# Performance work log

Measured on AMD Instinct MI355X. Metric: run time of the kernel, lower is better.

The kernel has to match this reference:

```python
import jax, jax.numpy as jnp
import numpy as np

NUM_HEADS = 12
QK_SCALE = 1.0
EPS = 1e-12  # torch.nn.functional.normalize default eps


def _l2norm(t):
    # matches torch F.normalize: x / max(||x||_2, eps) along last axis
    n = jnp.sqrt(jnp.sum(t * t, axis=-1, keepdims=True))
    return t / jnp.maximum(n, EPS)


def setup_inputs() -> dict:
    key = jax.random.key(0)
    k1, k2 = jax.random.split(key)
    B, N, dim = 8, 4096, 768
    x = jax.random.normal(k1, (B, N, 3 * dim), dtype=jnp.float32)
    temperature = jnp.ones((NUM_HEADS, 1, 1), dtype=jnp.float32)
    proj_w = jax.random.normal(k2, (dim, dim), dtype=jnp.float32) * (1.0 / np.sqrt(dim))
    proj_b = jnp.zeros((dim,), dtype=jnp.float32)
    return {"x": x, "temperature": temperature, "proj_w": proj_w, "proj_b": proj_b}


def reference(x, temperature, proj_w, proj_b):
    B, N, C3 = x.shape
    C = C3 // 3
    H = NUM_HEADS
    d = C // H
    # (B, N, 3, H, d) -> (3, B, H, N, d)
    qkv = x.reshape(B, N, 3, H, d).transpose(2, 0, 3, 1, 4)
    q, k, v = qkv[0], qkv[1], qkv[2]
    q = jnp.swapaxes(q, -2, -1) * QK_SCALE   # [B, H, d, N]
    v = jnp.swapaxes(v, -2, -1)              # [B, H, d, N]
    q = _l2norm(q)                           # normalize over tokens N
    k = _l2norm(k)                           # normalize over head dim d (k is [B,H,N,d])
    # cross-covariance attention over channels: [B, H, d, d]
    attn = jnp.einsum('bhdn,bhne->bhde', q, k) * temperature
    attn = jax.nn.softmax(attn, axis=-1)
    out = jnp.einsum('bhde,bhen->bhdn', attn, v)  # [B, H, d, N]
    out = out.transpose(0, 3, 1, 2).reshape(B, N, C)  # [B, N, C]
    out = out @ proj_w.T + proj_b
    return out
```

## Files before the change

### kernel.cpp

```cpp
#include <hip/hip_runtime.h>
#include <hip/hip_bf16.h>

#define BB 8
#define NN 4096
#define HH 12
#define CC 768
#define C3 2304

typedef float  f32x4  __attribute__((ext_vector_type(4)));
typedef __bf16 bf16x8 __attribute__((ext_vector_type(8)));
typedef __bf16 bf16x4 __attribute__((ext_vector_type(4)));

__device__ __forceinline__ void gload16(const void* g, void* l) {
  __builtin_amdgcn_global_load_lds((const __attribute__((address_space(1))) void*)g,
                                   (__attribute__((address_space(3))) void*)l, 16, 0, 0);
}

__global__ __launch_bounds__(256) void k1_logits(const float* __restrict__ x,
                                                 __bf16* __restrict__ vb,
                                                 float* __restrict__ Spart,
                                                 float* __restrict__ Qpart) {
  const int slice = blockIdx.x;
  const int h = blockIdx.y, b = blockIdx.z;
  const int tid = threadIdx.x;
  __shared__ __bf16 qT[64][40];
  __shared__ __bf16 kT[64][40];
  __shared__ float  qws[4][64];

  const int t   = tid >> 3;
  const int sub = tid & 7;
  const int w   = tid >> 6, lane = tid & 63;
  const int fr  = lane & 15, fk = lane >> 4;

  const float* qbase = x + (size_t)(b * NN + slice * 512) * C3 + h * 64 + sub * 8;
  __bf16* vbase = vb + (size_t)(b * NN + slice * 512) * CC + h * 64 + sub * 8;

  float qss8[8];
#pragma unroll
  for (int j = 0; j < 8; ++j) qss8[j] = 0.f;
  f32x4 acc[4];
#pragma unroll
  for (int tn = 0; tn < 4; ++tn) acc[tn] = (f32x4){0.f, 0.f, 0.f, 0.f};

  for (int step = 0; step < 16; ++step) {
    const float* qp = qbase + (size_t)(step * 32 + t) * C3;
    const float4 q0 = *(const float4*)(qp);
    const float4 q1 = *(const float4*)(qp + 4);
    const float4 k0 = *(const float4*)(qp + 768);
    const float4 k1 = *(const float4*)(qp + 772);
    const float4 v0 = *(const float4*)(qp + 1536);
    const float4 v1 = *(const float4*)(qp + 1540);
    float ss = k0.x * k0.x + k0.y * k0.y + k0.z * k0.z + k0.w * k0.w +
               k1.x * k1.x + k1.y * k1.y + k1.z * k1.z + k1.w * k1.w;
    ss += __shfl_xor(ss, 1);
    ss += __shfl_xor(ss, 2);
    ss += __shfl_xor(ss, 4);
    const float inv = 1.0f / fmaxf(sqrtf(ss), 1e-12f);
    bf16x8 vv;
    vv[0] = (__bf16)v0.x; vv[1] = (__bf16)v0.y; vv[2] = (__bf16)v0.z; vv[3] = (__bf16)v0.w;
    vv[4] = (__bf16)v1.x; vv[5] = (__bf16)v1.y; vv[6] = (__bf16)v1.z; vv[7] = (__bf16)v1.w;
    *(bf16x8*)(vbase + (size_t)(step * 32 + t) * CC) = vv;
    __syncthreads();
    const int c0 = sub * 8;
    qT[c0 + 0][t] = (__bf16)q0.x; qT[c0 + 1][t] = (__bf16)q0.y;
    qT[c0 + 2][t] = (__bf16)q0.z; qT[c0 + 3][t] = (__bf16)q0.w;
    qT[c0 + 4][t] = (__bf16)q1.x; qT[c0 + 5][t] = (__bf16)q1.y;
    qT[c0 + 6][t] = (__bf16)q1.z; qT[c0 + 7][t] = (__bf16)q1.w;
    kT[c0 + 0][t] = (__bf16)(k0.x * inv); kT[c0 + 1][t] = (__bf16)(k0.y * inv);
    kT[c0 + 2][t] = (__bf16)(k0.z * inv); kT[c0 + 3][t] = (__bf16)(k0.w * inv);
    kT[c0 + 4][t] = (__bf16)(k1.x * inv); kT[c0 + 5][t] = (__bf16)(k1.y * inv);
    kT[c0 + 6][t] = (__bf16)(k1.z * inv); kT[c0 + 7][t] = (__bf16)(k1.w * inv);
    qss8[0] = fmaf(q0.x, q0.x, qss8[0]); qss8[1] = fmaf(q0.y, q0.y, qss8[1]);
    qss8[2] = fmaf(q0.z, q0.z, qss8[2]); qss8[3] = fmaf(q0.w, q0.w, qss8[3]);
    qss8[4] = fmaf(q1.x, q1.x, qss8[4]); qss8[5] = fmaf(q1.y, q1.y, qss8[5]);
    qss8[6] = fmaf(q1.z, q1.z, qss8[6]); qss8[7] = fmaf(q1.w, q1.w, qss8[7]);
    __syncthreads();
    const bf16x8 afr = *(const bf16x8*)&qT[w * 16 + fr][fk * 8];
#pragma unroll
    for (int tn = 0; tn < 4; ++tn) {
      const bf16x8 bfr = *(const bf16x8*)&kT[tn * 16 + fr][fk * 8];
      acc[tn] = __builtin_amdgcn_mfma_f32_16x16x32_bf16(afr, bfr, acc[tn], 0, 0, 0);
    }
  }

  const int bh = b * HH + h;
  float* Sp = Spart + ((size_t)(slice * 96 + bh)) * 4096;
#pragma unroll
  for (int tn = 0; tn < 4; ++tn)
#pragma unroll
    for (int rr = 0; rr < 4; ++rr)
      Sp[(w * 16 + fk * 4 + rr) * 64 + tn * 16 + fr] = acc[tn][rr];

#pragma unroll
  for (int j = 0; j < 8; ++j) {
    float v = qss8[j];
    v += __shfl_xor(v, 8);
    v += __shfl_xor(v, 16);
    v += __shfl_xor(v, 32);
    if (lane < 8) qws[w][lane * 8 + j] = v;
  }
  __syncthreads();
  if (tid < 64) {
    const float qs = qws[0][tid] + qws[1][tid] + qws[2][tid] + qws[3][tid];
    Qpart[((size_t)(slice * 96 + bh)) * 64 + tid] = qs;
  }
}

__global__ __launch_bounds__(256) void k2_softmax(const float* __restrict__ Spart,
                                                  const float* __restrict__ Qpart,
                                                  const float* __restrict__ temp,
                                                  float* __restrict__ attn) {
  const int h = blockIdx.x, b = blockIdx.y;
  const int tid = threadIdx.x;
  const int i  = tid >> 2;
  const int qq = tid & 3;
  const int bh = b * HH + h;
  float qs = 0.f;
#pragma unroll
  for (int s = 0; s < 8; ++s) qs += Qpart[((size_t)(s * 96 + bh)) * 64 + i];
  float v[16];
#pragma unroll
  for (int j = 0; j < 16; ++j) v[j] = 0.f;
  for (int s = 0; s < 8; ++s) {
    const float* Sp = Spart + ((size_t)(s * 96 + bh)) * 4096 + i * 64 + qq * 16;
#pragma unroll
    for (int j = 0; j < 16; j += 4) {
      const float4 t4 = *(const float4*)(Sp + j);
      v[j] += t4.x; v[j + 1] += t4.y; v[j + 2] += t4.z; v[j + 3] += t4.w;
    }
  }
  const float rqs = 1.0f / fmaxf(sqrtf(qs), 1e-12f);
  const float tp  = temp[h] * rqs;
  float m = -3.4e38f;
#pragma unroll
  for (int j = 0; j < 16; ++j) { v[j] *= tp; m = fmaxf(m, v[j]); }
  m = fmaxf(m, __shfl_xor(m, 1));
  m = fmaxf(m, __shfl_xor(m, 2));
  float s = 0.f;
#pragma unroll
  for (int j = 0; j < 16; ++j) { v[j] = __expf(v[j] - m); s += v[j]; }
  s += __shfl_xor(s, 1);
  s += __shfl_xor(s, 2);
  const float inv = 1.0f / s;
  float* Ap = attn + (size_t)bh * 4096 + i * 64 + qq * 16;
#pragma unroll
  for (int j = 0; j < 16; j += 4) {
    float4 o;
    o.x = v[j] * inv; o.y = v[j + 1] * inv; o.z = v[j + 2] * inv; o.w = v[j + 3] * inv;
    *(float4*)(Ap + j) = o;
  }
}

__global__ __launch_bounds__(256) void k3_w2(const float* __restrict__ attn,
                                             const float* __restrict__ pw,
                                             __bf16* __restrict__ W2) {
  const int ct = blockIdx.x, h = blockIdx.y, b = blockIdx.z;
  const int co0 = ct * 64;
  __shared__ float pT[64][65];
  __shared__ float ab[64][64];
  const int tid = threadIdx.x;
  const int r = tid >> 2, c0 = (tid & 3) * 16;
  {
    const float* pp = pw + (size_t)(co0 + r) * CC + h * 64 + c0;
    const float4 p0 = *(const float4*)(pp + 0);
    const float4 p1 = *(const float4*)(pp + 4);
    const float4 p2 = *(const float4*)(pp + 8);
    const float4 p3 = *(const float4*)(pp + 12);
    const float* ap = attn + (size_t)(b * HH + h) * 4096 + r * 64 + c0;
    const float4 a0 = *(const float4*)(ap + 0);
    const float4 a1 = *(const float4*)(ap + 4);
    const float4 a2 = *(const float4*)(ap + 8);
    const float4 a3 = *(const float4*)(ap + 12);
    pT[c0 +  0][r] = p0.x; pT[c0 +  1][r] = p0.y; pT[c0 +  2][r] = p0.z; pT[c0 +  3][r] = p0.w;
    pT[c0 +  4][r] = p1.x; pT[c0 +  5][r] = p1.y; pT[c0 +  6][r] = p1.z; pT[c0 +  7][r] = p1.w;
    pT[c0 +  8][r] = p2.x; pT[c0 +  9][r] = p2.y; pT[c0 + 10][r] = p2.z; pT[c0 + 11][r] = p2.w;
    pT[c0 + 12][r] = p3.x; pT[c0 + 13][r] = p3.y; pT[c0 + 14][r] = p3.z; pT[c0 + 15][r] = p3.w;
    *(float4*)&ab[r][c0 + 0]  = a0;
    *(float4*)&ab[r][c0 + 4]  = a1;
    *(float4*)&ab[r][c0 + 8]  = a2;
    *(float4*)&ab[r][c0 + 12] = a3;
  }
  __syncthreads();
  const int col = tid & 63, jg = tid >> 6;
  float accJ[16];
#pragma unroll
  for (int c = 0; c < 16; ++c) accJ[c] = 0.f;
#pragma unroll 4
  for (int i = 0; i < 64; ++i) {
    const float p = pT[i][col];
    const float4* a4 = (const float4*)&ab[i][jg * 16];
    const float4 A0 = a4[0], A1 = a4[1], A2 = a4[2], A3 = a4[3];
    accJ[0]  = fmaf(p, A0.x, accJ[0]);  accJ[1]  = fmaf(p, A0.y, accJ[1]);
    accJ[2]  = fmaf(p, A0.z, accJ[2]);  accJ[3]  = fmaf(p, A0.w, accJ[3]);
    accJ[4]  = fmaf(p, A1.x, accJ[4]);  accJ[5]  = fmaf(p, A1.y, accJ[5]);
    accJ[6]  = fmaf(p, A1.z, accJ[6]);  accJ[7]  = fmaf(p, A1.w, accJ[7]);
    accJ[8]  = fmaf(p, A2.x, accJ[8]);  accJ[9]  = fmaf(p, A2.y, accJ[9]);
    accJ[10] = fmaf(p, A2.z, accJ[10]); accJ[11] = fmaf(p, A2.w, accJ[11]);
    accJ[12] = fmaf(p, A3.x, accJ[12]); accJ[13] = fmaf(p, A3.y, accJ[13]);
    accJ[14] = fmaf(p, A3.z, accJ[14]); accJ[15] = fmaf(p, A3.w, accJ[15]);
  }
  bf16x8 u0, u1;
#pragma unroll
  for (int c = 0; c < 8; ++c) { u0[c] = (__bf16)accJ[c]; u1[c] = (__bf16)accJ[8 + c]; }
  __bf16* wp = W2 + ((size_t)b * CC + co0 + col) * CC + h * 64 + jg * 16;
  *(bf16x8*)(wp)     = u0;
  *(bf16x8*)(wp + 8) = u1;
}

__global__ __launch_bounds__(256) void k4_gemm(const __bf16* __restrict__ vb,
                                               const __bf16* __restrict__ W2,
                                               const float* __restrict__ pb,
                                               float* __restrict__ out) {
  int id = blockIdx.x;
  const int bz = id / 192;
  const int rem = id - bz * 192;
  const int mg = rem / 48;
  const int idx = rem - mg * 48;
  const int nt = idx >> 3;
  const int mt = mg * 8 + (idx & 7);
  const int m0 = mt * 128, co0 = nt * 128;

  __shared__ __bf16 At[128][32];
  __shared__ __bf16 Bt[128][32];

  const int tid  = threadIdx.x;
  const int w    = tid >> 6, lane = tid & 63;
  const int wm   = w >> 1,   wn   = w & 1;
  const int fr   = lane & 15;
  const int fk   = lane >> 4;

  f32x4 acc[4][4];
#pragma unroll
  for (int tm = 0; tm < 4; ++tm)
#pragma unroll
    for (int tn = 0; tn < 4; ++tn) acc[tm][tn] = (f32x4){0.f, 0.f, 0.f, 0.f};

  const int srow = lane >> 2;
  const int scol = (lane & 3) * 8;
  const __bf16* Ag = vb + (size_t)(bz * NN + m0 + w * 32 + srow) * CC + scol;
  const __bf16* Bg = W2 + ((size_t)bz * CC + co0 + w * 32 + srow) * CC + scol;
  __bf16* lA0 = &At[w * 32][0];
  __bf16* lA1 = &At[w * 32 + 16][0];
  __bf16* lB0 = &Bt[w * 32][0];
  __bf16* lB1 = &Bt[w * 32 + 16][0];

  for (int kk = 0; kk < 24; ++kk) {
    const int kb = kk * 32;
    __syncthreads();
    gload16(Ag + kb,            lA0);
    gload16(Ag + 16 * CC + kb,  lA1);
    gload16(Bg + kb,            lB0);
    gload16(Bg + 16 * CC + kb,  lB1);
    __syncthreads();
    bf16x8 afr[4], bfr[4];
#pragma unroll
    for (int tm = 0; tm < 4; ++tm)
      afr[tm] = *(const bf16x8*)&At[wm * 64 + tm * 16 + fr][fk * 8];
#pragma unroll
    for (int tn = 0; tn < 4; ++tn)
      bfr[tn] = *(const bf16x8*)&Bt[wn * 64 + tn * 16 + fr][fk * 8];
#pragma unroll
    for (int tm = 0; tm < 4; ++tm)
#pragma unroll
      for (int tn = 0; tn < 4; ++tn)
        acc[tm][tn] = __builtin_amdgcn_mfma_f32_16x16x32_bf16(afr[tm], bfr[tn],
                                                              acc[tm][tn], 0, 0, 0);
  }

#pragma unroll
  for (int tn = 0; tn < 4; ++tn) {
    const int co = co0 + wn * 64 + tn * 16 + fr;
    const float bias = pb[co];
#pragma unroll
    for (int tm = 0; tm < 4; ++tm) {
#pragma unroll
      for (int rr = 0; rr < 4; ++rr) {
        const int row = m0 + wm * 64 + tm * 16 + fk * 4 + rr;
        out[(size_t)(bz * NN + row) * CC + co] = acc[tm][tn][rr] + bias;
      }
    }
  }
}

extern "C" void kernel_launch(void* const* d_in, const int* in_sizes, int n_in,
                              void* d_out, int out_size, void* d_ws, size_t ws_size,
                              hipStream_t stream) {
  const float* x    = (const float*)d_in[0];
  const float* temp = (const float*)d_in[1];
  const float* pw   = (const float*)d_in[2];
  const float* pb   = (const float*)d_in[3];
  float* out = (float*)d_out;
  char* ws = (char*)d_ws;

  float*  Spart = (float*)(ws);
  float*  Qpart = (float*)(ws + 12582912);
  float*  attn  = (float*)(ws + 12779520);
  __bf16* W2    = (__bf16*)(ws + 14352384);
  __bf16* vb    = (__bf16*)(ws + 23789568);

  hipLaunchKernelGGL(k1_logits,  dim3(8, 12, 8),  dim3(256), 0, stream, x, vb, Spart, Qpart);
  hipLaunchKernelGGL(k2_softmax, dim3(12, 8),     dim3(256), 0, stream, Spart, Qpart, temp, attn);
  hipLaunchKernelGGL(k3_w2,      dim3(12, 12, 8), dim3(256), 0, stream, attn, pw, W2);
  hipLaunchKernelGGL(k4_gemm,    dim3(1536),      dim3(256), 0, stream, vb, W2, pb, out);
}
```

Before: 531.5 us.

## Double-buffer q/k staging in logits kernel and split tokens into more slices

The logits kernel now double-buffers the transposed q/k tiles in LDS and prefetches the next step's global loads while the MFMAs run on the current buffer, which halves the barriers per step. The token range per block drops from 512 to 256, doubling the grid to 16 slices for more parallelism. The V bf16 conversion is moved into a separate loop at the end. The softmax kernel is widened to 512 threads to reduce the larger set of 16 partials, and the workspace offsets grow to hold them. The cost is more partial-sum traffic and a separate pass over V.

```diff
diff --git a/kernel.cpp b/kernel.cpp
--- a/kernel.cpp
+++ b/kernel.cpp
@@ -23,17 +23,17 @@
   const int slice = blockIdx.x;
   const int h = blockIdx.y, b = blockIdx.z;
   const int tid = threadIdx.x;
-  __shared__ __bf16 qT[64][40];
-  __shared__ __bf16 kT[64][40];
+  __shared__ __bf16 qT[2][64][40];
+  __shared__ __bf16 kT[2][64][40];
   __shared__ float  qws[4][64];
 
   const int t   = tid >> 3;
   const int sub = tid & 7;
   const int w   = tid >> 6, lane = tid & 63;
   const int fr  = lane & 15, fk = lane >> 4;
-
-  const float* qbase = x + (size_t)(b * NN + slice * 512) * C3 + h * 64 + sub * 8;
-  __bf16* vbase = vb + (size_t)(b * NN + slice * 512) * CC + h * 64 + sub * 8;
+  const int c0  = sub * 8;
+
+  const float* qbase = x + (size_t)(b * NN + slice * 256) * C3 + h * 64 + c0;
 
   float qss8[8];
 #pragma unroll
@@ -42,45 +42,75 @@
 #pragma unroll
   for (int tn = 0; tn < 4; ++tn) acc[tn] = (f32x4){0.f, 0.f, 0.f, 0.f};
 
-  for (int step = 0; step < 16; ++step) {
-    const float* qp = qbase + (size_t)(step * 32 + t) * C3;
+  {
+    const float* qp = qbase + (size_t)t * C3;
     const float4 q0 = *(const float4*)(qp);
     const float4 q1 = *(const float4*)(qp + 4);
     const float4 k0 = *(const float4*)(qp + 768);
     const float4 k1 = *(const float4*)(qp + 772);
-    const float4 v0 = *(const float4*)(qp + 1536);
-    const float4 v1 = *(const float4*)(qp + 1540);
     float ss = k0.x * k0.x + k0.y * k0.y + k0.z * k0.z + k0.w * k0.w +
                k1.x * k1.x + k1.y * k1.y + k1.z * k1.z + k1.w * k1.w;
     ss += __shfl_xor(ss, 1);
     ss += __shfl_xor(ss, 2);
     ss += __shfl_xor(ss, 4);
     const float inv = 1.0f / fmaxf(sqrtf(ss), 1e-12f);
-    bf16x8 vv;
-    vv[0] = (__bf16)v0.x; vv[1] = (__bf16)v0.y; vv[2] = (__bf16)v0.z; vv[3] = (__bf16)v0.w;
-    vv[4] = (__bf16)v1.x; vv[5] = (__bf16)v1.y; vv[6] = (__bf16)v1.z; vv[7] = (__bf16)v1.w;
-    *(bf16x8*)(vbase + (size_t)(step * 32 + t) * CC) = vv;
-    __syncthreads();
-    const int c0 = sub * 8;
-    qT[c0 + 0][t] = (__bf16)q0.x; qT[c0 + 1][t] = (__bf16)q0.y;
-    qT[c0 + 2][t] = (__bf16)q0.z; qT[c0 + 3][t] = (__bf16)q0.w;
-    qT[c0 + 4][t] = (__bf16)q1.x; qT[c0 + 5][t] = (__bf16)q1.y;
-    qT[c0 + 6][t] = (__bf16)q1.z; qT[c0 + 7][t] = (__bf16)q1.w;
-    kT[c0 + 0][t] = (__bf16)(k0.x * inv); kT[c0 + 1][t] = (__bf16)(k0.y * inv);
-    kT[c0 + 2][t] = (__bf16)(k0.z * inv); kT[c0 + 3][t] = (__bf16)(k0.w * inv);
-    kT[c0 + 4][t] = (__bf16)(k1.x * inv); kT[c0 + 5][t] = (__bf16)(k1.y * inv);
-    kT[c0 + 6][t] = (__bf16)(k1.z * inv); kT[c0 + 7][t] = (__bf16)(k1.w * inv);
+    qT[0][c0 + 0][t] = (__bf16)q0.x; qT[0][c0 + 1][t] = (__bf16)q0.y;
+    qT[0][c0 + 2][t] = (__bf16)q0.z; qT[0][c0 + 3][t] = (__bf16)q0.w;
+    qT[0][c0 + 4][t] = (__bf16)q1.x; qT[0][c0 + 5][t] = (__bf16)q1.y;
+    qT[0][c0 + 6][t] = (__bf16)q1.z; qT[0][c0 + 7][t] = (__bf16)q1.w;
+    kT[0][c0 + 0][t] = (__bf16)(k0.x * inv); kT[0][c0 + 1][t] = (__bf16)(k0.y * inv);
+    kT[0][c0 + 2][t] = (__bf16)(k0.z * inv); kT[0][c0 + 3][t] = (__bf16)(k0.w * inv);
+    kT[0][c0 + 4][t] = (__bf16)(k1.x * inv); kT[0][c0 + 5][t] = (__bf16)(k1.y * inv);
+    kT[0][c0 + 6][t] = (__bf16)(k1.z * inv); kT[0][c0 + 7][t] = (__bf16)(k1.w * inv);
     qss8[0] = fmaf(q0.x, q0.x, qss8[0]); qss8[1] = fmaf(q0.y, q0.y, qss8[1]);
     qss8[2] = fmaf(q0.z, q0.z, qss8[2]); qss8[3] = fmaf(q0.w, q0.w, qss8[3]);
     qss8[4] = fmaf(q1.x, q1.x, qss8[4]); qss8[5] = fmaf(q1.y, q1.y, qss8[5]);
     qss8[6] = fmaf(q1.z, q1.z, qss8[6]); qss8[7] = fmaf(q1.w, q1.w, qss8[7]);
+  }
+  __syncthreads();
+
+#pragma unroll
+  for (int step = 0; step < 8; ++step) {
+    const int cur = step & 1;
+    float4 q0, q1, k0, k1;
+    if (step < 7) {
+      const float* np = qbase + (size_t)((step + 1) * 32 + t) * C3;
+      q0 = *(const float4*)(np);
+      q1 = *(const float4*)(np + 4);
+      k0 = *(const float4*)(np + 768);
+      k1 = *(const float4*)(np + 772);
+    }
+    const bf16x8 afr = *(const bf16x8*)&qT[cur][w * 16 + fr][fk * 8];
+    const bf16x8 b0 = *(const bf16x8*)&kT[cur][0 * 16 + fr][fk * 8];
+    const bf16x8 b1 = *(const bf16x8*)&kT[cur][1 * 16 + fr][fk * 8];
+    const bf16x8 b2 = *(const bf16x8*)&kT[cur][2 * 16 + fr][fk * 8];
+    const bf16x8 b3 = *(const bf16x8*)&kT[cur][3 * 16 + fr][fk * 8];
+    acc[0] = __builtin_amdgcn_mfma_f32_16x16x32_bf16(afr, b0, acc[0], 0, 0, 0);
+    acc[1] = __builtin_amdgcn_mfma_f32_16x16x32_bf16(afr, b1, acc[1], 0, 0, 0);
+    acc[2] = __builtin_amdgcn_mfma_f32_16x16x32_bf16(afr, b2, acc[2], 0, 0, 0);
+    acc[3] = __builtin_amdgcn_mfma_f32_16x16x32_bf16(afr, b3, acc[3], 0, 0, 0);
+    if (step < 7) {
+      const int nxt = cur ^ 1;
+      float ss = k0.x * k0.x + k0.y * k0.y + k0.z * k0.z + k0.w * k0.w +
+                 k1.x * k1.x + k1.y * k1.y + k1.z * k1.z + k1.w * k1.w;
+      ss += __shfl_xor(ss, 1);
+      ss += __shfl_xor(ss, 2);
+      ss += __shfl_xor(ss, 4);
+      const float inv = 1.0f / fmaxf(sqrtf(ss), 1e-12f);
+      qT[nxt][c0 + 0][t] = (__bf16)q0.x; qT[nxt][c0 + 1][t] = (__bf16)q0.y;
+      qT[nxt][c0 + 2][t] = (__bf16)q0.z; qT[nxt][c0 + 3][t] = (__bf16)q0.w;
+      qT[nxt][c0 + 4][t] = (__bf16)q1.x; qT[nxt][c0 + 5][t] = (__bf16)q1.y;
+      qT[nxt][c0 + 6][t] = (__bf16)q1.z; qT[nxt][c0 + 7][t] = (__bf16)q1.w;
+      kT[nxt][c0 + 0][t] = (__bf16)(k0.x * inv); kT[nxt][c0 + 1][t] = (__bf16)(k0.y * inv);
+      kT[nxt][c0 + 2][t] = (__bf16)(k0.z * inv); kT[nxt][c0 + 3][t] = (__bf16)(k0.w * inv);
+      kT[nxt][c0 + 4][t] = (__bf16)(k1.x * inv); kT[nxt][c0 + 5][t] = (__bf16)(k1.y * inv);
+      kT[nxt][c0 + 6][t] = (__bf16)(k1.z * inv); kT[nxt][c0 + 7][t] = (__bf16)(k1.w * inv);
+      qss8[0] = fmaf(q0.x, q0.x, qss8[0]); qss8[1] = fmaf(q0.y, q0.y, qss8[1]);
+      qss8[2] = fmaf(q0.z, q0.z, qss8[2]); qss8[3] = fmaf(q0.w, q0.w, qss8[3]);
+      qss8[4] = fmaf(q1.x, q1.x, qss8[4]); qss8[5] = fmaf(q1.y, q1.y, qss8[5]);
+      qss8[6] = fmaf(q1.z, q1.z, qss8[6]); qss8[7] = fmaf(q1.w, q1.w, qss8[7]);
+    }
     __syncthreads();
-    const bf16x8 afr = *(const bf16x8*)&qT[w * 16 + fr][fk * 8];
-#pragma unroll
-    for (int tn = 0; tn < 4; ++tn) {
-      const bf16x8 bfr = *(const bf16x8*)&kT[tn * 16 + fr][fk * 8];
-      acc[tn] = __builtin_amdgcn_mfma_f32_16x16x32_bf16(afr, bfr, acc[tn], 0, 0, 0);
-    }
   }
 
   const int bh = b * HH + h;
@@ -104,51 +134,65 @@
     const float qs = qws[0][tid] + qws[1][tid] + qws[2][tid] + qws[3][tid];
     Qpart[((size_t)(slice * 96 + bh)) * 64 + tid] = qs;
   }
-}
-
-__global__ __launch_bounds__(256) void k2_softmax(const float* __restrict__ Spart,
+
+  const float* vsrc = x + (size_t)(b * NN + slice * 256) * C3 + 1536 + h * 64 + c0;
+  __bf16* vdst = vb + (size_t)(b * NN + slice * 256) * CC + h * 64 + c0;
+#pragma unroll
+  for (int r = 0; r < 8; ++r) {
+    const size_t tok = (size_t)(r * 32 + t);
+    const float4 v0 = *(const float4*)(vsrc + tok * C3);
+    const float4 v1 = *(const float4*)(vsrc + tok * C3 + 4);
+    bf16x8 vv;
+    vv[0] = (__bf16)v0.x; vv[1] = (__bf16)v0.y; vv[2] = (__bf16)v0.z; vv[3] = (__bf16)v0.w;
+    vv[4] = (__bf16)v1.x; vv[5] = (__bf16)v1.y; vv[6] = (__bf16)v1.z; vv[7] = (__bf16)v1.w;
+    *(bf16x8*)(vdst + tok * CC) = vv;
+  }
+}
+
+__global__ __launch_bounds__(512) void k2_softmax(const float* __restrict__ Spart,
                                                   const float* __restrict__ Qpart,
                                                   const float* __restrict__ temp,
                                                   float* __restrict__ attn) {
   const int h = blockIdx.x, b = blockIdx.y;
   const int tid = threadIdx.x;
-  const int i  = tid >> 2;
-  const int qq = tid & 3;
+  const int i = tid >> 3;
+  const int g = tid & 7;
   const int bh = b * HH + h;
   float qs = 0.f;
 #pragma unroll
-  for (int s = 0; s < 8; ++s) qs += Qpart[((size_t)(s * 96 + bh)) * 64 + i];
-  float v[16];
-#pragma unroll
-  for (int j = 0; j < 16; ++j) v[j] = 0.f;
-  for (int s = 0; s < 8; ++s) {
-    const float* Sp = Spart + ((size_t)(s * 96 + bh)) * 4096 + i * 64 + qq * 16;
-#pragma unroll
-    for (int j = 0; j < 16; j += 4) {
-      const float4 t4 = *(const float4*)(Sp + j);
-      v[j] += t4.x; v[j + 1] += t4.y; v[j + 2] += t4.z; v[j + 3] += t4.w;
-    }
+  for (int s = 0; s < 16; ++s) qs += Qpart[((size_t)(s * 96 + bh)) * 64 + i];
+  float v[8];
+#pragma unroll
+  for (int j = 0; j < 8; ++j) v[j] = 0.f;
+#pragma unroll 4
+  for (int s = 0; s < 16; ++s) {
+    const float* Sp = Spart + ((size_t)(s * 96 + bh)) * 4096 + i * 64 + g * 8;
+    const float4 t0 = *(const float4*)(Sp);
+    const float4 t1 = *(const float4*)(Sp + 4);
+    v[0] += t0.x; v[1] += t0.y; v[2] += t0.z; v[3] += t0.w;
+    v[4] += t1.x; v[5] += t1.y; v[6] += t1.z; v[7] += t1.w;
   }
   const float rqs = 1.0f / fmaxf(sqrtf(qs), 1e-12f);
   const float tp  = temp[h] * rqs;
   float m = -3.4e38f;
 #pragma unroll
-  for (int j = 0; j < 16; ++j) { v[j] *= tp; m = fmaxf(m, v[j]); }
+  for (int j = 0; j < 8; ++j) { v[j] *= tp; m = fmaxf(m, v[j]); }
   m = fmaxf(m, __shfl_xor(m, 1));
   m = fmaxf(m, __shfl_xor(m, 2));
+  m = fmaxf(m, __shfl_xor(m, 4));
   float s = 0.f;
 #pragma unroll
-  for (int j = 0; j < 16; ++j) { v[j] = __expf(v[j] - m); s += v[j]; }
+  for (int j = 0; j < 8; ++j) { v[j] = __expf(v[j] - m); s += v[j]; }
   s += __shfl_xor(s, 1);
   s += __shfl_xor(s, 2);
+  s += __shfl_xor(s, 4);
   const float inv = 1.0f / s;
-  float* Ap = attn + (size_t)bh * 4096 + i * 64 + qq * 16;
-#pragma unroll
-  for (int j = 0; j < 16; j += 4) {
-    float4 o;
-    o.x = v[j] * inv; o.y = v[j + 1] * inv; o.z = v[j + 2] * inv; o.w = v[j + 3] * inv;
-    *(float4*)(Ap + j) = o;
-  }
+  float* Ap = attn + (size_t)bh * 4096 + i * 64 + g * 8;
+  float4 o0, o1;
+  o0.x = v[0] * inv; o0.y = v[1] * inv; o0.z = v[2] * inv; o0.w = v[3] * inv;
+  o1.x = v[4] * inv; o1.y = v[5] * inv; o1.z = v[6] * inv; o1.w = v[7] * inv;
+  *(float4*)(Ap)     = o0;
+  *(float4*)(Ap + 4) = o1;
 }
 
 __global__ __launch_bounds__(256) void k3_w2(const float* __restrict__ attn,
@@ -293,13 +337,13 @@
   char* ws = (char*)d_ws;
 
   float*  Spart = (float*)(ws);
-  float*  Qpart = (float*)(ws + 12582912);
-  float*  attn  = (float*)(ws + 12779520);
-  __bf16* W2    = (__bf16*)(ws + 14352384);
-  __bf16* vb    = (__bf16*)(ws + 23789568);
-
-  hipLaunchKernelGGL(k1_logits,  dim3(8, 12, 8),  dim3(256), 0, stream, x, vb, Spart, Qpart);
-  hipLaunchKernelGGL(k2_softmax, dim3(12, 8),     dim3(256), 0, stream, Spart, Qpart, temp, attn);
+  float*  Qpart = (float*)(ws + 25165824);
+  float*  attn  = (float*)(ws + 25559040);
+  __bf16* W2    = (__bf16*)(ws + 27131904);
+  __bf16* vb    = (__bf16*)(ws + 36569088);
+
+  hipLaunchKernelGGL(k1_logits,  dim3(16, 12, 8), dim3(256), 0, stream, x, vb, Spart, Qpart);
+  hipLaunchKernelGGL(k2_softmax, dim3(12, 8),     dim3(512), 0, stream, Spart, Qpart, temp, attn);
   hipLaunchKernelGGL(k3_w2,      dim3(12, 12, 8), dim3(256), 0, stream, attn, pw, W2);
   hipLaunchKernelGGL(k4_gemm,    dim3(1536),      dim3(256), 0, stream, vb, W2, pb, out);
 }
```

Measured after the change: 521.9 us. No clear change (-1.8%).
